# Optimization experiments

Measured on AMD Instinct MI355X. Metric: run time of the kernel, lower is better.

Reference implementation:

```python
import jax, jax.numpy as jnp
import numpy as np

P = 3; Q = 3                 # spline degrees (deg_p, deg_q)
OUT_U = 64; OUT_V = 64       # surface evaluation grid
W_CTRL = 1.0; W_SURF = 1.0
B = 1024; MU_MAX = 32; MV_MAX = 32
EPS = 1e-5                   # SurfEval samples u,v in [eps, 1-eps]


def _open_uniform_knots(n_valid, degree, n_max):
    """Clamped open-uniform knot vector for n_valid ctrl pts, padded to static
    length n_max+degree+1. Entries beyond the valid span are clamped to 1.0,
    which makes the padded basis functions identically zero on [eps, 1-eps]."""
    L = n_valid + degree + 1  # true (ragged) knot count, traced int
    k = jnp.arange(n_max + degree + 1)
    interior = k.astype(jnp.float32) / (L - 1).astype(jnp.float32)
    return jnp.where(k <= degree, 0.0, jnp.where(k >= L - 1 - degree, 1.0, interior))


def _bspline_basis(kv, degree, u):
    """Cox-de Boor, vectorized over u. kv: (n_max+degree+1,), u: (U,).
    Returns (U, n_max) basis matrix; padded columns are exactly zero."""
    N = ((u[None, :] >= kv[:-1, None]) & (u[None, :] < kv[1:, None])).astype(jnp.float32)
    for d in range(1, degree + 1):
        m = N.shape[0] - 1  # number of basis funcs at this level
        den1 = kv[d:d + m] - kv[:m]
        den2 = kv[d + 1:d + 1 + m] - kv[1:1 + m]
        s1 = jnp.where((den1 > 0)[:, None],
                       (u[None, :] - kv[:m, None]) / jnp.where(den1 > 0, den1, 1.0)[:, None], 0.0)
        s2 = jnp.where((den2 > 0)[:, None],
                       (kv[d + 1:d + 1 + m, None] - u[None, :]) / jnp.where(den2 > 0, den2, 1.0)[:, None], 0.0)
        N = s1 * N[:m] + s2 * N[1:m + 1]
    return N.T  # (U, n_max)


def _eval_surface(ctrl, mask_b, u, v):
    """NURBS surface eval for one sample with ragged (Mu_i, Mv_i) via padded
    knots/basis; unit weights => rational division by basis partition sum."""
    mu = jnp.maximum(jnp.sum(jnp.any(mask_b > 0, axis=1)), P + 1)
    mv = jnp.maximum(jnp.sum(jnp.any(mask_b > 0, axis=0)), Q + 1)
    Bu = _bspline_basis(_open_uniform_knots(mu, P, MU_MAX), P, u)  # (OUT_U, MU_MAX)
    Bv = _bspline_basis(_open_uniform_knots(mv, Q, MV_MAX), Q, v)  # (OUT_V, MV_MAX)
    num = jnp.einsum('ui,vj,ijd->uvd', Bu, Bv, ctrl)               # (OUT_U, OUT_V, 3)
    den = Bu.sum(-1)[:, None] * Bv.sum(-1)[None, :]                # unit-weight denom
    return num / den[..., None]


def setup_inputs() -> dict:
    key = jax.random.key(0)
    k1, k2, k3, k4, k5 = jax.random.split(key, 5)
    # ragged true control sizes per sample, >= degree+1
    mu = jax.random.randint(k1, (B,), P + 1, MU_MAX + 1)
    mv = jax.random.randint(k2, (B,), Q + 1, MV_MAX + 1)
    mask = ((jnp.arange(MU_MAX)[None, :, None] < mu[:, None, None]) &
            (jnp.arange(MV_MAX)[None, None, :] < mv[:, None, None])).astype(jnp.float32)
    ctrl_pred_pad = jax.random.normal(k3, (B, MU_MAX, MV_MAX, 3), jnp.float32)
    ctrl_gt_pad = jax.random.normal(k4, (B, MU_MAX, MV_MAX, 3), jnp.float32)
    xyz_samples = jax.random.normal(k5, (B, OUT_U, OUT_V, 3), jnp.float32)
    return {"ctrl_pred_pad": ctrl_pred_pad, "ctrl_gt_pad": ctrl_gt_pad,
            "mask": mask, "xyz_samples": xyz_samples}


def reference(ctrl_pred_pad, ctrl_gt_pad, mask, xyz_samples):
    # masked control-point MSE
    diff2 = ((ctrl_pred_pad - ctrl_gt_pad) ** 2).sum(-1)
    loss_ctrl = (diff2 * mask).sum() / jnp.maximum(mask.sum() * 3.0, 1.0)
    # batched ragged surface evaluation
    u = jnp.linspace(EPS, 1.0 - EPS, OUT_U)
    v = jnp.linspace(EPS, 1.0 - EPS, OUT_V)
    surf = jax.vmap(lambda c, m: _eval_surface(c, m, u, v))(ctrl_pred_pad, mask)
    loss_surf = jnp.mean((surf.reshape(B, -1, 3) - xyz_samples.reshape(B, -1, 3)) ** 2)
    total = W_CTRL * loss_ctrl + W_SURF * loss_surf  # original computes total BEFORE nan-guard
    bad = jnp.isnan(surf).any() | jnp.isinf(surf).any()
    surf_mse = jnp.where(bad, jnp.float32(1e6), loss_surf)
    return total, loss_ctrl, surf_mse
```

## Files before the change

### kernel.cpp

```cpp
#include <hip/hip_runtime.h>
#include <math.h>

#define MU_MAXC 32
#define MV_MAXC 32
#define OUT_UC  64
#define OUT_VC  64
#define DEG     3
#define NKNOT   (MU_MAXC + DEG + 1)
#define EPSV    1e-5f

__global__ void zero_ws_kernel(double* acc, int* bad) {
    acc[0] = 0.0; acc[1] = 0.0; acc[2] = 0.0; bad[0] = 0;
}

template <int MODE>
__launch_bounds__(256, 5)
__global__ void nurbs_loss_kernel(const float* __restrict__ ctrl_pred,
                                  const float* __restrict__ ctrl_gt,
                                  const float* __restrict__ mask,
                                  const float* __restrict__ xyz,
                                  double* __restrict__ pd, int Bcnt,
                                  int* __restrict__ badp)
{
    const int b   = blockIdx.x;
    const int tid = threadIdx.x;

    __shared__ float s_tmp[OUT_UC * MV_MAXC * 3];
    __shared__ float s_Bu4[4 * OUT_UC];
    __shared__ float s_Bv4[4 * OUT_VC];
    __shared__ int   s_uoff[OUT_UC];
    __shared__ int   s_voff[OUT_VC];
    __shared__ float s_sumBu[OUT_UC];
    __shared__ float s_sumBv[OUT_VC];
    __shared__ float s_knots_u[NKNOT];
    __shared__ float s_knots_v[NKNOT];
    __shared__ int   s_rowany[MU_MAXC];
    __shared__ int   s_colany[MV_MAXC];
    __shared__ int   s_mu, s_mv, s_bad;
    __shared__ float s_wred[4], s_wred2[4];
    __shared__ float s_ctrl_diff, s_ctrl_mask;

    if (tid < 32) { s_rowany[tid] = 0; s_colany[tid] = 0; }
    if (tid == 0) s_bad = 0;
    __syncthreads();

    float lsum_mask = 0.f, lsum_diff = 0.f;
    for (int k = 0; k < 4; k++) {
        const int cell = tid + 256 * k;
        const int base = (b * 1024 + cell) * 3;
        const float m  = mask[b * 1024 + cell];
        const float p0 = ctrl_pred[base + 0], p1 = ctrl_pred[base + 1], p2 = ctrl_pred[base + 2];
        const float g0 = ctrl_gt[base + 0],   g1 = ctrl_gt[base + 1],   g2 = ctrl_gt[base + 2];
        const float d0 = p0 - g0, d1 = p1 - g1, d2 = p2 - g2;
        lsum_mask += m;
        lsum_diff += m * (d0 * d0 + d1 * d1 + d2 * d2);
        if (m > 0.f) { s_rowany[cell >> 5] = 1; s_colany[cell & 31] = 1; }
    }
    #pragma unroll
    for (int off = 32; off > 0; off >>= 1) {
        lsum_mask += __shfl_down(lsum_mask, off);
        lsum_diff += __shfl_down(lsum_diff, off);
    }
    if ((tid & 63) == 0) { s_wred[tid >> 6] = lsum_mask; s_wred2[tid >> 6] = lsum_diff; }
    __syncthreads();

    if (tid == 0) {
        int cu = 0, cv = 0;
        #pragma unroll
        for (int i = 0; i < 32; i++) { cu += s_rowany[i]; cv += s_colany[i]; }
        s_mu = cu > (DEG + 1) ? cu : (DEG + 1);
        s_mv = cv > (DEG + 1) ? cv : (DEG + 1);
        s_ctrl_mask = s_wred[0] + s_wred[1] + s_wred[2] + s_wred[3];
        s_ctrl_diff = s_wred2[0] + s_wred2[1] + s_wred2[2] + s_wred2[3];
    }
    __syncthreads();

    if (tid < NKNOT) {
        const int L = s_mu + DEG + 1;
        s_knots_u[tid] = (tid <= DEG) ? 0.f
                        : ((tid >= L - 1 - DEG) ? 1.f : (float)tid / (float)(L - 1));
    } else if (tid >= 64 && tid < 64 + NKNOT) {
        const int k = tid - 64;
        const int L = s_mv + DEG + 1;
        s_knots_v[k] = (k <= DEG) ? 0.f
                      : ((k >= L - 1 - DEG) ? 1.f : (float)k / (float)(L - 1));
    }
    __syncthreads();

    if (tid < 128) {
        const bool isU = tid < 64;
        const int t = isU ? tid : (tid - 64);
        const float* kv = isU ? s_knots_u : s_knots_v;
        const float step = (1.f - 2.f * EPSV) / 63.f;
        const float uu = (t == 63) ? (1.f - EPSV) : (EPSV + step * (float)t);

        int span = DEG;
        #pragma unroll
        for (int k = DEG + 1; k < NKNOT - 1; k++)
            if (kv[k] <= uu) span = k;

        float N4[DEG + 1], left[DEG + 1], right[DEG + 1];
        N4[0] = 1.f;
        #pragma unroll
        for (int j = 1; j <= DEG; j++) {
            left[j]  = uu - kv[span + 1 - j];
            right[j] = kv[span + j] - uu;
            float saved = 0.f;
            #pragma unroll
            for (int r = 0; r < j; r++) {
                const float temp = N4[r] / (right[r + 1] + left[j - r]);
                N4[r] = saved + right[r + 1] * temp;
                saved = left[j - r] * temp;
            }
            N4[j] = saved;
        }
        const float s = N4[0] + N4[1] + N4[2] + N4[3];
        const int off = span - DEG;
        if (isU) {
            #pragma unroll
            for (int r = 0; r < 4; r++) s_Bu4[r * 64 + t] = N4[r];
            s_uoff[t] = off; s_sumBu[t] = s;
        } else {
            #pragma unroll
            for (int r = 0; r < 4; r++) s_Bv4[r * 64 + t] = N4[r];
            s_voff[t] = off; s_sumBv[t] = s;
        }
    }
    __syncthreads();

    const float* ctrlb = ctrl_pred + (size_t)b * 1024 * 3;
    for (int k = 0; k < 24; k++) {
        const int flat = tid + 256 * k;
        const int u = flat / 96;
        const int jd = flat - u * 96;
        const int off = s_uoff[u];
        float a = 0.f;
        #pragma unroll
        for (int r = 0; r < 4; r++)
            a += s_Bu4[r * 64 + u] * ctrlb[(off + r) * 96 + jd];
        s_tmp[flat] = a;
    }
    __syncthreads();

    float lsum_surf = 0.f;
    int bad = 0;
    for (int k = 0; k < 16; k++) {
        const int p = tid + 256 * k;
        const int u = p >> 6, v = p & 63;
        const float* tp = &s_tmp[u * 96 + s_voff[v] * 3];
        float n0 = 0.f, n1 = 0.f, n2 = 0.f;
        #pragma unroll
        for (int r = 0; r < 4; r++) {
            const float w = s_Bv4[r * 64 + v];
            n0 += w * tp[r * 3 + 0];
            n1 += w * tp[r * 3 + 1];
            n2 += w * tp[r * 3 + 2];
        }
        const float inv = 1.0f / (s_sumBu[u] * s_sumBv[v]);
        const float x0 = n0 * inv, x1 = n1 * inv, x2 = n2 * inv;
        const int base = (b * 4096 + p) * 3;
        const float d0 = x0 - xyz[base + 0];
        const float d1 = x1 - xyz[base + 1];
        const float d2 = x2 - xyz[base + 2];
        lsum_surf += d0 * d0 + d1 * d1 + d2 * d2;
        if (!isfinite(x0) || !isfinite(x1) || !isfinite(x2)) bad = 1;
    }
    #pragma unroll
    for (int off = 32; off > 0; off >>= 1)
        lsum_surf += __shfl_down(lsum_surf, off);
    if ((tid & 63) == 0) s_wred[tid >> 6] = lsum_surf;
    if (bad) atomicOr(&s_bad, 1);
    __syncthreads();

    if (tid == 0) {
        const double surf = (double)s_wred[0] + s_wred[1] + s_wred[2] + s_wred[3];
        if (MODE == 0) {
            pd[b]             = (double)s_ctrl_diff;
            pd[Bcnt + b]      = (double)s_ctrl_mask;
            pd[2 * Bcnt + b]  = surf;
            badp[b]           = s_bad;
        } else {
            atomicAdd(&pd[0], (double)s_ctrl_diff);
            atomicAdd(&pd[1], (double)s_ctrl_mask);
            atomicAdd(&pd[2], surf);
            if (s_bad) atomicOr(badp, 1);
        }
    }
}

__global__ void finalize_partials_kernel(const double* __restrict__ pd,
                                         const int* __restrict__ badp,
                                         float* __restrict__ out, int Bcnt)
{
    __shared__ double sd0[4], sd1[4], sd2[4];
    __shared__ int sb[4];
    const int tid = threadIdx.x;
    double a0 = 0.0, a1 = 0.0, a2 = 0.0; int bad = 0;
    for (int i = tid; i < Bcnt; i += 256) {
        a0 += pd[i]; a1 += pd[Bcnt + i]; a2 += pd[2 * Bcnt + i];
        bad |= badp[i];
    }
    #pragma unroll
    for (int off = 32; off > 0; off >>= 1) {
        a0 += __shfl_down(a0, off);
        a1 += __shfl_down(a1, off);
        a2 += __shfl_down(a2, off);
        bad |= __shfl_down(bad, off);
    }
    if ((tid & 63) == 0) { const int w = tid >> 6; sd0[w] = a0; sd1[w] = a1; sd2[w] = a2; sb[w] = bad; }
    __syncthreads();
    if (tid == 0) {
        double d0 = 0, d1 = 0, d2 = 0; int bb = 0;
        #pragma unroll
        for (int i = 0; i < 4; i++) { d0 += sd0[i]; d1 += sd1[i]; d2 += sd2[i]; bb |= sb[i]; }
        const double denc = d1 * 3.0;
        const double lc = d0 / (denc > 1.0 ? denc : 1.0);
        const double ls = d2 / ((double)Bcnt * OUT_UC * OUT_VC * 3.0);
        out[0] = (float)(lc + ls);
        out[1] = (float)lc;
        out[2] = bb ? 1.0e6f : (float)ls;
    }
}

__global__ void finalize_atomic_kernel(const double* __restrict__ acc,
                                       const int* __restrict__ bad,
                                       float* __restrict__ out, int Bcnt)
{
    const double denc = acc[1] * 3.0;
    const double lc = acc[0] / (denc > 1.0 ? denc : 1.0);
    const double ls = acc[2] / ((double)Bcnt * OUT_UC * OUT_VC * 3.0);
    out[0] = (float)(lc + ls);
    out[1] = (float)lc;
    out[2] = bad[0] ? 1.0e6f : (float)ls;
}

extern "C" void kernel_launch(void* const* d_in, const int* in_sizes, int n_in,
                              void* d_out, int out_size, void* d_ws, size_t ws_size,
                              hipStream_t stream)
{
    const float* pred = (const float*)d_in[0];
    const float* gt   = (const float*)d_in[1];
    const float* mask = (const float*)d_in[2];
    const float* xyz  = (const float*)d_in[3];
    const int Bcnt = in_sizes[2] / (MU_MAXC * MV_MAXC);

    double* pd = (double*)d_ws;
    float* out = (float*)d_out;

    const size_t need = (size_t)3 * Bcnt * sizeof(double) + (size_t)Bcnt * sizeof(int);
    if (ws_size >= need) {
        int* badp = (int*)(pd + 3 * Bcnt);
        hipLaunchKernelGGL((nurbs_loss_kernel<0>), dim3(Bcnt), dim3(256), 0, stream,
                           pred, gt, mask, xyz, pd, Bcnt, badp);
        hipLaunchKernelGGL(finalize_partials_kernel, dim3(1), dim3(256), 0, stream,
                           pd, badp, out, Bcnt);
    } else {
        int* badp = (int*)(pd + 3);
        hipLaunchKernelGGL(zero_ws_kernel, dim3(1), dim3(1), 0, stream, pd, badp);
        hipLaunchKernelGGL((nurbs_loss_kernel<1>), dim3(Bcnt), dim3(256), 0, stream,
                           pred, gt, mask, xyz, pd, Bcnt, badp);
        hipLaunchKernelGGL(finalize_atomic_kernel, dim3(1), dim3(1), 0, stream,
                           pd, badp, out, Bcnt);
    }
}
```

Measured before the change: 115.2 us.

## Vectorize ctrl loads as float4, hoist v-basis weights, precompute reciprocal sums

Stages the mask in shared memory so the control-point MSE can read pred and gt as contiguous float4 loads instead of strided scalar triples. The u-direction contraction also uses float4 loads and writes. The v-basis weights and offset are hoisted out of the surface loop, since each thread now keeps a fixed v column. The per-point divide is replaced by precomputed reciprocals, with 1/sumBv folded into the Bv weights. This cuts global load instructions and per-point arithmetic, at the cost of 4KB more shared memory, which may lower occupancy, and slightly different rounding from the folded reciprocal.

```diff
diff --git a/kernel.cpp b/kernel.cpp
--- a/kernel.cpp
+++ b/kernel.cpp
@@ -26,12 +26,12 @@
     const int tid = threadIdx.x;
 
     __shared__ float s_tmp[OUT_UC * MV_MAXC * 3];
+    __shared__ float s_mask[1024];
     __shared__ float s_Bu4[4 * OUT_UC];
     __shared__ float s_Bv4[4 * OUT_VC];
     __shared__ int   s_uoff[OUT_UC];
     __shared__ int   s_voff[OUT_VC];
-    __shared__ float s_sumBu[OUT_UC];
-    __shared__ float s_sumBv[OUT_VC];
+    __shared__ float s_invSumBu[OUT_UC];
     __shared__ float s_knots_u[NKNOT];
     __shared__ float s_knots_v[NKNOT];
     __shared__ int   s_rowany[MU_MAXC];
@@ -44,17 +44,33 @@
     if (tid == 0) s_bad = 0;
     __syncthreads();
 
-    float lsum_mask = 0.f, lsum_diff = 0.f;
+    float lsum_mask = 0.f;
+    #pragma unroll
     for (int k = 0; k < 4; k++) {
         const int cell = tid + 256 * k;
-        const int base = (b * 1024 + cell) * 3;
         const float m  = mask[b * 1024 + cell];
-        const float p0 = ctrl_pred[base + 0], p1 = ctrl_pred[base + 1], p2 = ctrl_pred[base + 2];
-        const float g0 = ctrl_gt[base + 0],   g1 = ctrl_gt[base + 1],   g2 = ctrl_gt[base + 2];
-        const float d0 = p0 - g0, d1 = p1 - g1, d2 = p2 - g2;
+        s_mask[cell] = m;
         lsum_mask += m;
-        lsum_diff += m * (d0 * d0 + d1 * d1 + d2 * d2);
         if (m > 0.f) { s_rowany[cell >> 5] = 1; s_colany[cell & 31] = 1; }
+    }
+    __syncthreads();
+
+    float lsum_diff = 0.f;
+    {
+        const float4* p4 = (const float4*)(ctrl_pred + (size_t)b * 3072);
+        const float4* g4 = (const float4*)(ctrl_gt   + (size_t)b * 3072);
+        #pragma unroll
+        for (int k = 0; k < 3; k++) {
+            const int e4 = tid + 256 * k;
+            const float4 p = p4[e4];
+            const float4 g = g4[e4];
+            const int e = e4 * 4;
+            const float dx = p.x - g.x, dy = p.y - g.y, dz = p.z - g.z, dw = p.w - g.w;
+            lsum_diff += s_mask[(e + 0) / 3] * dx * dx
+                       + s_mask[(e + 1) / 3] * dy * dy
+                       + s_mask[(e + 2) / 3] * dz * dz
+                       + s_mask[(e + 3) / 3] * dw * dw;
+        }
     }
     #pragma unroll
     for (int off = 32; off > 0; off >>= 1) {
@@ -115,55 +131,72 @@
             N4[j] = saved;
         }
         const float s = N4[0] + N4[1] + N4[2] + N4[3];
+        const float invs = 1.0f / s;
         const int off = span - DEG;
         if (isU) {
             #pragma unroll
             for (int r = 0; r < 4; r++) s_Bu4[r * 64 + t] = N4[r];
-            s_uoff[t] = off; s_sumBu[t] = s;
+            s_uoff[t] = off; s_invSumBu[t] = invs;
         } else {
             #pragma unroll
-            for (int r = 0; r < 4; r++) s_Bv4[r * 64 + t] = N4[r];
-            s_voff[t] = off; s_sumBv[t] = s;
-        }
-    }
-    __syncthreads();
-
-    const float* ctrlb = ctrl_pred + (size_t)b * 1024 * 3;
-    for (int k = 0; k < 24; k++) {
-        const int flat = tid + 256 * k;
-        const int u = flat / 96;
-        const int jd = flat - u * 96;
-        const int off = s_uoff[u];
-        float a = 0.f;
-        #pragma unroll
-        for (int r = 0; r < 4; r++)
-            a += s_Bu4[r * 64 + u] * ctrlb[(off + r) * 96 + jd];
-        s_tmp[flat] = a;
+            for (int r = 0; r < 4; r++) s_Bv4[r * 64 + t] = N4[r] * invs;
+            s_voff[t] = off;
+        }
+    }
+    __syncthreads();
+
+    {
+        const float4* ctrl4 = (const float4*)(ctrl_pred + (size_t)b * 3072);
+        float4* tmp4 = (float4*)s_tmp;
+        #pragma unroll
+        for (int k = 0; k < 6; k++) {
+            const int flat4 = tid + 256 * k;
+            const int u = flat4 / 24;
+            const int q = flat4 - u * 24;
+            const int off = s_uoff[u];
+            const float w0 = s_Bu4[0 * 64 + u];
+            const float w1 = s_Bu4[1 * 64 + u];
+            const float w2 = s_Bu4[2 * 64 + u];
+            const float w3 = s_Bu4[3 * 64 + u];
+            const float4 c0 = ctrl4[(off + 0) * 24 + q];
+            const float4 c1 = ctrl4[(off + 1) * 24 + q];
+            const float4 c2 = ctrl4[(off + 2) * 24 + q];
+            const float4 c3 = ctrl4[(off + 3) * 24 + q];
+            float4 a;
+            a.x = w0 * c0.x + w1 * c1.x + w2 * c2.x + w3 * c3.x;
+            a.y = w0 * c0.y + w1 * c1.y + w2 * c2.y + w3 * c3.y;
+            a.z = w0 * c0.z + w1 * c1.z + w2 * c2.z + w3 * c3.z;
+            a.w = w0 * c0.w + w1 * c1.w + w2 * c2.w + w3 * c3.w;
+            tmp4[flat4] = a;
+        }
     }
     __syncthreads();
 
     float lsum_surf = 0.f;
     int bad = 0;
-    for (int k = 0; k < 16; k++) {
-        const int p = tid + 256 * k;
-        const int u = p >> 6, v = p & 63;
-        const float* tp = &s_tmp[u * 96 + s_voff[v] * 3];
-        float n0 = 0.f, n1 = 0.f, n2 = 0.f;
-        #pragma unroll
-        for (int r = 0; r < 4; r++) {
-            const float w = s_Bv4[r * 64 + v];
-            n0 += w * tp[r * 3 + 0];
-            n1 += w * tp[r * 3 + 1];
-            n2 += w * tp[r * 3 + 2];
-        }
-        const float inv = 1.0f / (s_sumBu[u] * s_sumBv[v]);
-        const float x0 = n0 * inv, x1 = n1 * inv, x2 = n2 * inv;
-        const int base = (b * 4096 + p) * 3;
-        const float d0 = x0 - xyz[base + 0];
-        const float d1 = x1 - xyz[base + 1];
-        const float d2 = x2 - xyz[base + 2];
-        lsum_surf += d0 * d0 + d1 * d1 + d2 * d2;
-        if (!isfinite(x0) || !isfinite(x1) || !isfinite(x2)) bad = 1;
+    {
+        const int v = tid & 63;
+        const int voff3 = s_voff[v] * 3;
+        const float w0 = s_Bv4[0 * 64 + v];
+        const float w1 = s_Bv4[1 * 64 + v];
+        const float w2 = s_Bv4[2 * 64 + v];
+        const float w3 = s_Bv4[3 * 64 + v];
+        #pragma unroll
+        for (int k = 0; k < 16; k++) {
+            const int u = (tid >> 6) + 4 * k;
+            const float* tp = &s_tmp[u * 96 + voff3];
+            const float n0 = w0 * tp[0] + w1 * tp[3] + w2 * tp[6] + w3 * tp[9];
+            const float n1 = w0 * tp[1] + w1 * tp[4] + w2 * tp[7] + w3 * tp[10];
+            const float n2 = w0 * tp[2] + w1 * tp[5] + w2 * tp[8] + w3 * tp[11];
+            const float inv = s_invSumBu[u];
+            const float x0 = n0 * inv, x1 = n1 * inv, x2 = n2 * inv;
+            const int base = (b * 4096 + u * 64 + v) * 3;
+            const float d0 = x0 - xyz[base + 0];
+            const float d1 = x1 - xyz[base + 1];
+            const float d2 = x2 - xyz[base + 2];
+            lsum_surf += d0 * d0 + d1 * d1 + d2 * d2;
+            if (!isfinite(x0) || !isfinite(x1) || !isfinite(x2)) bad = 1;
+        }
     }
     #pragma unroll
     for (int off = 32; off > 0; off >>= 1)
```

New measurement: 178.4 us. +54.9%, slower.
